# Kernel optimization log

Measured on AMD Instinct MI355X. Metric: run time of the kernel, lower is better.

## Reference

```python
import jax, jax.numpy as jnp
import numpy as np

BETA = 100.0
# (in_ch, out_ch) for the 12 effective 1x1-conv layers. ResNeXt blocks are
# fused: all branches read the same block input, so stacking branch weights
# along out-channels gives one GEMM per block.
LAYER_DIMS = [(259, 515), (515, 512), (512, 512), (512, 576), (576, 576),
              (576, 768), (768, 768), (768, 768), (768, 960), (960, 960),
              (960, 896), (896, 1)]


def setup_inputs() -> dict:
    key = jax.random.key(0)
    keys = jax.random.split(key, 2 + len(LAYER_DIMS))
    B, N = 2, 8192
    inp = {
        "input": jax.random.normal(keys[0], (B, N, 3), dtype=jnp.float32),
        "latent": jax.random.normal(keys[1], (B, 256), dtype=jnp.float32),
    }
    for i, (cin, cout) in enumerate(LAYER_DIMS):
        std = np.sqrt(2.0) / np.sqrt(cin)
        inp[f"W{i+1}"] = std * jax.random.normal(keys[2 + i], (cout, cin), dtype=jnp.float32)
        inp[f"b{i+1}"] = jnp.zeros((cout,), dtype=jnp.float32)
    return inp


def _sp(z):
    # torch Softplus(beta=100): softplus(beta*z)/beta (jax.nn.softplus is stable)
    return jax.nn.softplus(BETA * z) / BETA


def reference(input, latent,
              W1, b1, W2, b2, W3, b3, W4, b4, W5, b5, W6, b6,
              W7, b7, W8, b8, W9, b9, W10, b10, W11, b11, W12, b12):
    B, N, _ = input.shape
    lat = jnp.broadcast_to(latent[:, None, :], (B, N, latent.shape[-1]))
    x = jnp.concatenate([input, lat], axis=-1)  # (B, N, 259)
    input_con = x

    # layer 1: conv + softplus, grad seeded from first 3 input columns (xyz)
    z = x @ W1.T + b1                                   # (B, N, 515)
    g = jax.nn.sigmoid(BETA * z)[..., None] * W1[:, :3]  # (B, N, 515, 3)
    x = _sp(z)

    mids = [(W2, b2), (W3, b3), (W4, b4), (W5, b5), (W6, b6), (W7, b7),
            (W8, b8), (W9, b9), (W10, b10), (W11, b11)]
    for W, b in mids:  # fixed small layer loop (10 fused ResNeXt blocks)
        z = x @ W.T + b                                 # (B, N, Cout)
        g = jax.nn.sigmoid(BETA * z)[..., None] * jnp.einsum('oc,bnci->bnoi', W, g)
        x = _sp(z)

    # final 1x1 conv, no activation
    z = x @ W12.T + b12                                 # (B, N, 1)
    g = jnp.einsum('oc,bnci->bnoi', W12, g)             # (B, N, 1, 3)
    # torch returns conv output channel-first: (B, 1, N)
    return (z.transpose(0, 2, 1), g, input_con)
```

## Files before the change

kernel.cpp:

```cpp
#include <hip/hip_runtime.h>
#include <math.h>


typedef unsigned short u16;
typedef _Float16 f16;
typedef f16   f16x8  __attribute__((ext_vector_type(8)));
typedef float f32x16 __attribute__((ext_vector_type(16)));

__device__ __forceinline__ u16   f2h(float x){ return __builtin_bit_cast(u16, (f16)x); }
__device__ __forceinline__ float h2f(u16 b){ return (float)__builtin_bit_cast(f16, b); }

__device__ __forceinline__ void glld16(const void* g, void* l){
  __builtin_amdgcn_global_load_lds(
      (const __attribute__((address_space(1))) unsigned*)g,
      (__attribute__((address_space(3))) unsigned*)l, 16, 0, 0);
}

template<int NP>
__global__ __launch_bounds__(256, 2)
void fused_layer(const u16* __restrict__ Sin, long long psIn, int kpad,
                 u16* __restrict__ Sout, long long psOut, int opitch,
                 const u16* __restrict__ Wh, const u16* __restrict__ Wl,
                 const float* __restrict__ bias, const float* __restrict__ Wfirst,
                 int cout, int cinFirst)
{
  constexpr bool FIRST = (NP == 2);
  __shared__ u16 As[2][NP][4][64][8];
  __shared__ u16 Bs[2][2][4][128][8];

  const int tid   = threadIdx.x;
  const int w     = tid >> 6;
  const int lane  = tid & 63;
  const int lrow  = lane & 31;
  const int lhalf = lane >> 5;
  const int mh    = w >> 1;
  const int oh    = w & 1;
  const int m0    = blockIdx.x * 64;
  const int o0    = blockIdx.y * 128;

  f32x16 zinit = {};
  f32x16 accx[2];
  f32x16 accg[FIRST ? 1 : 3][2];
  accx[0] = zinit; accx[1] = zinit;
  if constexpr (!FIRST){
    #pragma unroll
    for (int j = 0; j < 3; ++j){ accg[j][0] = zinit; accg[j][1] = zinit; }
  }

  const u16* aSrc[NP];
  #pragma unroll
  for (int p = 0; p < NP; ++p)
    aSrc[p] = Sin + (long long)p * psIn + (long long)(m0 + lane) * kpad + w * 8;
  const u16* bSrc[2][2];
  #pragma unroll
  for (int h = 0; h < 2; ++h){
    const u16* Wx = h ? Wl : Wh;
    #pragma unroll
    for (int hf = 0; hf < 2; ++hf)
      bSrc[h][hf] = Wx + (long long)(o0 + hf*64 + lane) * kpad + w * 8;
  }

  auto stage = [&](int cur, int kk){
    #pragma unroll
    for (int p = 0; p < NP; ++p)
      glld16(aSrc[p] + kk, &As[cur][p][w][0][0]);
    #pragma unroll
    for (int h = 0; h < 2; ++h)
      #pragma unroll
      for (int hf = 0; hf < 2; ++hf)
        glld16(bSrc[h][hf] + kk, &Bs[cur][h][w][hf*64][0]);
  };

  auto compute = [&](int cur){
    #pragma unroll
    for (int s = 0; s < 2; ++s){
      const int kq = s*2 + lhalf;
      f16x8 a[NP];
      #pragma unroll
      for (int p = 0; p < NP; ++p)
        a[p] = *(const f16x8*)&As[cur][p][kq][mh*32 + lrow][0];
      #pragma unroll
      for (int f = 0; f < 2; ++f){
        const int oc = oh*64 + f*32 + lrow;
        f16x8 bh = *(const f16x8*)&Bs[cur][0][kq][oc][0];
        f16x8 bl = *(const f16x8*)&Bs[cur][1][kq][oc][0];
        accx[f] = __builtin_amdgcn_mfma_f32_32x32x16_f16(a[0], bh, accx[f], 0,0,0);
        accx[f] = __builtin_amdgcn_mfma_f32_32x32x16_f16(a[1], bh, accx[f], 0,0,0);
        accx[f] = __builtin_amdgcn_mfma_f32_32x32x16_f16(a[0], bl, accx[f], 0,0,0);
        if constexpr (!FIRST){
          #pragma unroll
          for (int j = 0; j < 3; ++j)
            accg[j][f] = __builtin_amdgcn_mfma_f32_32x32x16_f16(a[2+j], bh, accg[j][f], 0,0,0);
        }
      }
    }
  };

  const int nk = kpad >> 5;
  stage(0, 0);
  __syncthreads();
  int cur = 0;
  for (int t = 1; t < nk; ++t){
    stage(cur ^ 1, t * 32);
    compute(cur);
    __syncthreads();
    cur ^= 1;
  }
  compute(cur);

  const int mb = m0 + mh*32;
  #pragma unroll
  for (int f = 0; f < 2; ++f){
    const int o = o0 + oh*64 + f*32 + lrow;
    const float bo = (o < cout) ? bias[o] : 0.f;
    float w0 = 0.f, w1 = 0.f, w2 = 0.f;
    if constexpr (FIRST){
      if (o < cout){
        w0 = Wfirst[(long long)o*cinFirst + 0];
        w1 = Wfirst[(long long)o*cinFirst + 1];
        w2 = Wfirst[(long long)o*cinFirst + 2];
      }
    }
    #pragma unroll
    for (int r = 0; r < 16; ++r){
      const int m = mb + (r & 3) + ((r >> 2) << 3) + (lhalf << 2);
      const float z    = accx[f][r] + bo;
      const float gate = 1.f / (1.f + expf(-100.f * z));
      const float sp   = fmaxf(z, 0.f) + 0.01f * log1pf(expf(-100.f * fabsf(z)));
      const long long idx = (long long)m * opitch + o;
      const u16 xh = f2h(sp);
      Sout[idx]          = xh;
      Sout[psOut + idx]  = f2h(sp - h2f(xh));
      if constexpr (FIRST){
        Sout[2*psOut + idx] = f2h(gate * w0);
        Sout[3*psOut + idx] = f2h(gate * w1);
        Sout[4*psOut + idx] = f2h(gate * w2);
      } else {
        Sout[2*psOut + idx] = f2h(gate * accg[0][f][r]);
        Sout[3*psOut + idx] = f2h(gate * accg[1][f][r]);
        Sout[4*psOut + idx] = f2h(gate * accg[2][f][r]);
      }
    }
  }
}

__global__ __launch_bounds__(256)
void final_layer(const u16* __restrict__ Sin, long long ps, int kpad,
                 const float* __restrict__ W, const float* __restrict__ bias,
                 float* __restrict__ out1, float* __restrict__ out2,
                 int cin, int mBase)
{
  const int lane = threadIdx.x & 63;
  const int wv   = threadIdx.x >> 6;
  const int m = blockIdx.x * 4 + wv;
  const u16* row = Sin + (long long)m * kpad;
  float s0=0.f, s1=0.f, s2=0.f, s3=0.f;
  for (int c = lane; c < cin; c += 64){
    const float w = W[c];
    s0 += (h2f(row[c]) + h2f(row[ps + c])) * w;
    s1 += h2f(row[2*ps + c]) * w;
    s2 += h2f(row[3*ps + c]) * w;
    s3 += h2f(row[4*ps + c]) * w;
  }
  #pragma unroll
  for (int off = 32; off > 0; off >>= 1){
    s0 += __shfl_xor(s0, off); s1 += __shfl_xor(s1, off);
    s2 += __shfl_xor(s2, off); s3 += __shfl_xor(s3, off);
  }
  if (lane == 0){
    out1[mBase + m] = s0 + bias[0];
    float* g = out2 + (long long)(mBase + m) * 3;
    g[0] = s1; g[1] = s2; g[2] = s3;
  }
}

__global__ void prep_input(const float* __restrict__ input,
                           const float* __restrict__ latent,
                           float* __restrict__ out3,
                           u16* __restrict__ x0, long long psX0, int N)
{
  const int m = blockIdx.x;
  const int b = m / N;
  const int c = threadIdx.x;
  if (c >= 288) return;
  float v = 0.f;
  if (c < 3) v = input[(long long)m*3 + c];
  else if (c < 259) v = latent[(long long)b*256 + (c - 3)];
  if (c < 259) out3[(long long)m*259 + c] = v;
  const u16 h = f2h(v);
  x0[(long long)m*288 + c]        = h;
  x0[psX0 + (long long)m*288 + c] = f2h(v - h2f(h));
}

__global__ void split_w(const float* __restrict__ W, u16* __restrict__ wh,
                        u16* __restrict__ wl, int cout, int cin, int kpad, int total)
{
  const int idx = blockIdx.x * 256 + threadIdx.x;
  if (idx >= total) return;
  const int o = idx / kpad, c = idx % kpad;
  const float v = (o < cout && c < cin) ? W[(long long)o*cin + c] : 0.f;
  const u16 h = f2h(v);
  wh[idx] = h;
  wl[idx] = f2h(v - h2f(h));
}

extern "C" void kernel_launch(void* const* d_in, const int* in_sizes, int n_in,
                              void* d_out, int out_size, void* d_ws, size_t ws_size,
                              hipStream_t stream)
{
  static const int CIN [12] = {259,515,512,512,576,576,768,768,768,960,960,896};
  static const int COUT[12] = {515,512,512,576,576,768,768,768,960,960,896,1};
  int OPAD[11], KPAD[12];
  KPAD[0] = 288;
  for (int i = 0; i < 11; ++i){
    OPAD[i] = ((COUT[i] + 127) / 128) * 128;
    KPAD[i+1] = OPAD[i];
  }

  const float* input  = (const float*)d_in[0];
  const float* latent = (const float*)d_in[1];
  auto Wp = [&](int i){ return (const float*)d_in[2 + 2*i]; };
  auto Bp = [&](int i){ return (const float*)d_in[3 + 2*i]; };

  const int Bn = in_sizes[1] / 256;
  const int Nn = in_sizes[0] / (3 * Bn);
  const int M  = Bn * Nn;

  float* out1 = (float*)d_out;
  float* out2 = out1 + M;
  float* out3 = out2 + (size_t)M * 3;

  char* wsp = (char*)d_ws;
  u16 *WH[11], *WL[11];
  for (int i = 0; i < 11; ++i){
    const size_t sz = (size_t)OPAD[i] * KPAD[i] * 2;
    WH[i] = (u16*)wsp; wsp += sz;
    WL[i] = (u16*)wsp; wsp += sz;
  }
  u16* x0 = (u16*)wsp;
  const long long psX0 = (long long)M * 288;
  wsp += (size_t)2 * psX0 * 2;

  const size_t used = (size_t)(wsp - (char*)d_ws);
  const size_t remain = (ws_size > used) ? (ws_size - used) : 0;
  const size_t perPoint = (size_t)2 * 5 * 1024 * 2;
  long long pc = (long long)(remain / perPoint);
  pc &= ~63LL;
  int Pc = (int)((pc < (long long)M) ? pc : (long long)M);
  if (Pc < 64) Pc = 64;
  u16* bufA = (u16*)wsp;
  u16* bufB = bufA + (size_t)5 * Pc * 1024;

  prep_input<<<M, 320, 0, stream>>>(input, latent, out3, x0, psX0, Nn);
  for (int i = 0; i < 11; ++i){
    const int total = OPAD[i] * KPAD[i];
    split_w<<<(total + 255)/256, 256, 0, stream>>>(
        Wp(i), WH[i], WL[i], COUT[i], CIN[i], KPAD[i], total);
  }

  for (int cm0 = 0; cm0 < M; cm0 += Pc){
    const int Mc = (M - cm0 < Pc) ? (M - cm0) : Pc;

    {
      dim3 g(Mc/64, OPAD[0]/128);
      fused_layer<2><<<g, 256, 0, stream>>>(
          x0 + (long long)cm0 * 288, psX0, 288,
          bufA, (long long)Pc * OPAD[0], OPAD[0],
          WH[0], WL[0], Bp(0), Wp(0), COUT[0], CIN[0]);
    }
    u16* src = bufA;
    u16* dst = bufB;
    for (int i = 1; i <= 10; ++i){
      dim3 g(Mc/64, OPAD[i]/128);
      fused_layer<5><<<g, 256, 0, stream>>>(
          src, (long long)Pc * KPAD[i], KPAD[i],
          dst, (long long)Pc * OPAD[i], OPAD[i],
          WH[i], WL[i], Bp(i), nullptr, COUT[i], 0);
      u16* t = src; src = dst; dst = t;
    }
    final_layer<<<Mc/4, 256, 0, stream>>>(
        src, (long long)Pc * KPAD[11], KPAD[11],
        Wp(11), Bp(11), out1, out2, CIN[11], cm0);
  }
}
```

Baseline: 3.162 ms.

## Deepen GEMM prefetch with vmcnt waits, swizzle workgroups, cap point chunk size

The main loop now prefetches two K-slices ahead and waits on vmcnt counts instead of a full __syncthreads, so global-to-LDS loads overlap compute more deeply. Compute sections are bracketed with s_setprio. Workgroup IDs are remapped in an XCD-aware interleave to improve cache locality across chiplets. The point-chunk size is capped at 8192 so intermediate activations are more likely to stay in cache, at the cost of more kernel launches. The hand-written waitcnt literals rely on an exact count of outstanding loads per stage, which is fragile if the load count changes.

```diff
diff --git a/kernel.cpp b/kernel.cpp
--- a/kernel.cpp
+++ b/kernel.cpp
@@ -14,6 +14,13 @@
   __builtin_amdgcn_global_load_lds(
       (const __attribute__((address_space(1))) unsigned*)g,
       (__attribute__((address_space(3))) unsigned*)l, 16, 0, 0);
+}
+
+template<int N> __device__ __forceinline__ void wait_vmcnt(){
+  static_assert(N == 0 || N == 6 || N == 9, "unsupported vmcnt literal");
+  if constexpr (N == 0) asm volatile("s_waitcnt vmcnt(0)" ::: "memory");
+  if constexpr (N == 6) asm volatile("s_waitcnt vmcnt(6)" ::: "memory");
+  if constexpr (N == 9) asm volatile("s_waitcnt vmcnt(9)" ::: "memory");
 }
 
 template<int NP>
@@ -25,8 +32,21 @@
                  int cout, int cinFirst)
 {
   constexpr bool FIRST = (NP == 2);
+  constexpr int  S     = NP + 4;
   __shared__ u16 As[2][NP][4][64][8];
   __shared__ u16 Bs[2][2][4][128][8];
+
+  int bx = blockIdx.x, by = blockIdx.y;
+  {
+    const int nwg = gridDim.x * gridDim.y;
+    const int d   = by * gridDim.x + bx;
+    if ((nwg & 7) == 0){
+      const int q = nwg >> 3;
+      const int r = (d & 7) * q + (d >> 3);
+      bx = r % gridDim.x;
+      by = r / gridDim.x;
+    }
+  }
 
   const int tid   = threadIdx.x;
   const int w     = tid >> 6;
@@ -35,8 +55,8 @@
   const int lhalf = lane >> 5;
   const int mh    = w >> 1;
   const int oh    = w & 1;
-  const int m0    = blockIdx.x * 64;
-  const int o0    = blockIdx.y * 128;
+  const int m0    = bx * 64;
+  const int o0    = by * 128;
 
   f32x16 zinit = {};
   f32x16 accx[2];
@@ -60,30 +80,31 @@
       bSrc[h][hf] = Wx + (long long)(o0 + hf*64 + lane) * kpad + w * 8;
   }
 
-  auto stage = [&](int cur, int kk){
+  auto stage = [&](int buf, int kElem){
     #pragma unroll
     for (int p = 0; p < NP; ++p)
-      glld16(aSrc[p] + kk, &As[cur][p][w][0][0]);
+      glld16(aSrc[p] + kElem, &As[buf][p][w][0][0]);
     #pragma unroll
     for (int h = 0; h < 2; ++h)
       #pragma unroll
       for (int hf = 0; hf < 2; ++hf)
-        glld16(bSrc[h][hf] + kk, &Bs[cur][h][w][hf*64][0]);
+        glld16(bSrc[h][hf] + kElem, &Bs[buf][h][w][hf*64][0]);
   };
 
-  auto compute = [&](int cur){
+  auto compute = [&](int buf){
+    __builtin_amdgcn_s_setprio(1);
     #pragma unroll
     for (int s = 0; s < 2; ++s){
       const int kq = s*2 + lhalf;
       f16x8 a[NP];
       #pragma unroll
       for (int p = 0; p < NP; ++p)
-        a[p] = *(const f16x8*)&As[cur][p][kq][mh*32 + lrow][0];
+        a[p] = *(const f16x8*)&As[buf][p][kq][mh*32 + lrow][0];
       #pragma unroll
       for (int f = 0; f < 2; ++f){
         const int oc = oh*64 + f*32 + lrow;
-        f16x8 bh = *(const f16x8*)&Bs[cur][0][kq][oc][0];
-        f16x8 bl = *(const f16x8*)&Bs[cur][1][kq][oc][0];
+        f16x8 bh = *(const f16x8*)&Bs[buf][0][kq][oc][0];
+        f16x8 bl = *(const f16x8*)&Bs[buf][1][kq][oc][0];
         accx[f] = __builtin_amdgcn_mfma_f32_32x32x16_f16(a[0], bh, accx[f], 0,0,0);
         accx[f] = __builtin_amdgcn_mfma_f32_32x32x16_f16(a[1], bh, accx[f], 0,0,0);
         accx[f] = __builtin_amdgcn_mfma_f32_32x32x16_f16(a[0], bl, accx[f], 0,0,0);
@@ -94,18 +115,24 @@
         }
       }
     }
+    __builtin_amdgcn_s_setprio(0);
   };
 
   const int nk = kpad >> 5;
   stage(0, 0);
-  __syncthreads();
+  stage(1, 32);
   int cur = 0;
-  for (int t = 1; t < nk; ++t){
-    stage(cur ^ 1, t * 32);
+  for (int t = 0; t < nk - 1; ++t){
+    wait_vmcnt<S>();
+    __builtin_amdgcn_s_barrier();
     compute(cur);
-    __syncthreads();
+    asm volatile("s_waitcnt lgkmcnt(0)" ::: "memory");
+    __builtin_amdgcn_s_barrier();
+    if (t + 2 < nk) stage(cur, (t + 2) * 32);
     cur ^= 1;
   }
+  wait_vmcnt<0>();
+  __builtin_amdgcn_s_barrier();
   compute(cur);
 
   const int mb = m0 + mh*32;
@@ -246,7 +273,8 @@
   const size_t perPoint = (size_t)2 * 5 * 1024 * 2;
   long long pc = (long long)(remain / perPoint);
   pc &= ~63LL;
-  int Pc = (int)((pc < (long long)M) ? pc : (long long)M);
+  int Pc = (int)((pc < 8192LL) ? pc : 8192LL);
+  if (Pc > M) Pc = M;
   if (Pc < 64) Pc = 64;
   u16* bufA = (u16*)wsp;
   u16* bufB = bufA + (size_t)5 * Pc * 1024;
```

Result: faster. 2.827 ms (-10.6%).
